# Kernel tuning notes

Measured on AMD Instinct MI355X. Metric: run time of the kernel, lower is better.

## Reference

```python
import jax, jax.numpy as jnp
import numpy as np

D, NH, NL, NP, DFF = 256, 8, 4, 4, 1024
HD = D // NH
SHAPES = np.array([[100, 152], [50, 76], [25, 38], [13, 19]], dtype=np.int64)
LV = int((SHAPES[:, 0] * SHAPES[:, 1]).sum())  # 20197


def setup_inputs() -> dict:
    key = jax.random.key(0)
    ks = iter(jax.random.split(key, 48))
    bs, Lq = 8, 300

    def w(shape, s=0.02):
        return jax.random.normal(next(ks), shape, jnp.float32) * s

    lsi = np.concatenate([[0], np.cumsum(SHAPES[:, 0] * SHAPES[:, 1])[:-1]]).astype(np.int64)
    return dict(
        tgt=w((bs, Lq, D), 1.0),
        query_pos=w((bs, Lq, D), 1.0),
        reference_points=jax.random.uniform(next(ks), (bs, Lq, NL, 2), jnp.float32),
        src=w((bs, LV, D), 1.0),
        in_proj_w=w((3 * D, D)), in_proj_b=jnp.zeros((3 * D,), jnp.float32),
        out_proj_w=w((D, D)), out_proj_b=jnp.zeros((D,), jnp.float32),
        samp_off_w=w((NH * NL * NP * 2, D)), samp_off_b=w((NH * NL * NP * 2,), 0.5),
        attn_w_w=w((NH * NL * NP, D)), attn_w_b=jnp.zeros((NH * NL * NP,), jnp.float32),
        value_proj_w=w((D, D)), value_proj_b=jnp.zeros((D,), jnp.float32),
        output_proj_w=w((D, D)), output_proj_b=jnp.zeros((D,), jnp.float32),
        lin1_w=w((DFF, D)), lin1_b=jnp.zeros((DFF,), jnp.float32),
        lin2_w=w((D, DFF)), lin2_b=jnp.zeros((D,), jnp.float32),
        norm1_w=jnp.ones((D,), jnp.float32), norm1_b=jnp.zeros((D,), jnp.float32),
        norm2_w=jnp.ones((D,), jnp.float32), norm2_b=jnp.zeros((D,), jnp.float32),
        norm3_w=jnp.ones((D,), jnp.float32), norm3_b=jnp.zeros((D,), jnp.float32),
        spatial_shapes=SHAPES,            # static numpy (shapes must be static)
        level_start_index=lsi,            # static numpy
        padding_mask=jnp.zeros((bs, LV), bool),
    )


def _ln(x, w, b):
    m = x.mean(-1, keepdims=True)
    v = ((x - m) ** 2).mean(-1, keepdims=True)
    return (x - m) * jax.lax.rsqrt(v + 1e-5) * w + b


def _bilinear(vflat, H_, W_, loc):
    # vflat: (b,h,H*W,d); loc: (b,h,q,p,2) normalized to [0,1]
    # matches F.grid_sample(align_corners=False, padding_mode='zeros')
    x = loc[..., 0] * W_ - 0.5
    y = loc[..., 1] * H_ - 0.5
    x0f, y0f = jnp.floor(x), jnp.floor(y)
    lx, ly = x - x0f, y - y0f
    x0, y0 = x0f.astype(jnp.int32), y0f.astype(jnp.int32)
    b, h, q, p = x0.shape

    def gather(ix, iy, wgt):
        valid = (ix >= 0) & (ix < W_) & (iy >= 0) & (iy < H_)
        idx = (jnp.clip(iy, 0, H_ - 1) * W_ + jnp.clip(ix, 0, W_ - 1)).reshape(b, h, q * p)
        g = jnp.take_along_axis(vflat, idx[..., None], axis=2)  # (b,h,q*p,d)
        return g * (wgt * valid).reshape(b, h, q * p, 1)

    out = (gather(x0, y0, (1 - lx) * (1 - ly)) + gather(x0 + 1, y0, lx * (1 - ly))
           + gather(x0, y0 + 1, (1 - lx) * ly) + gather(x0 + 1, y0 + 1, lx * ly))
    return out.reshape(b, h, q, p, -1)


def reference(tgt, query_pos, reference_points, src, in_proj_w, in_proj_b,
              out_proj_w, out_proj_b, samp_off_w, samp_off_b, attn_w_w, attn_w_b,
              value_proj_w, value_proj_b, output_proj_w, output_proj_b,
              lin1_w, lin1_b, lin2_w, lin2_b, norm1_w, norm1_b, norm2_w, norm2_b,
              norm3_w, norm3_b, spatial_shapes, level_start_index, padding_mask):
    bs, Lq, _ = tgt.shape
    ss = np.asarray(spatial_shapes)
    lsi = np.asarray(level_start_index)

    # ---- self attention (eval mode, dropout off) ----
    qk = tgt + query_pos
    qh = (qk @ in_proj_w[:D].T + in_proj_b[:D]).reshape(bs, Lq, NH, HD)
    kh = (qk @ in_proj_w[D:2 * D].T + in_proj_b[D:2 * D]).reshape(bs, Lq, NH, HD)
    vh = (tgt @ in_proj_w[2 * D:].T + in_proj_b[2 * D:]).reshape(bs, Lq, NH, HD)
    scores = jnp.einsum('bqhd,bkhd->bhqk', qh, kh) / jnp.sqrt(jnp.float32(HD))
    attn = jax.nn.softmax(scores, axis=-1)
    sa = jnp.einsum('bhqk,bkhd->bqhd', attn, vh).reshape(bs, Lq, D)
    sa = sa @ out_proj_w.T + out_proj_b
    x = _ln(tgt + sa, norm2_w, norm2_b)

    # ---- MSDeformAttn cross attention ----
    query = x + query_pos
    value = src @ value_proj_w.T + value_proj_b
    value = jnp.where(padding_mask[..., None], 0.0, value)
    value_t = value.reshape(bs, -1, NH, HD).transpose(0, 2, 1, 3)  # (b,h,Lv,d)

    offsets = (query @ samp_off_w.T + samp_off_b).reshape(bs, Lq, NH, NL, NP, 2)
    aw = jax.nn.softmax((query @ attn_w_w.T + attn_w_b).reshape(bs, Lq, NH, NL * NP), -1)
    aw = aw.reshape(bs, Lq, NH, NL, NP)
    norma = jnp.asarray(np.stack([ss[:, 1], ss[:, 0]], -1), jnp.float32)  # (NL,2)=[W,H]
    loc = reference_points[:, :, None, :, None, :] + offsets / norma[None, None, None, :, None, :]

    out = jnp.zeros((bs, Lq, NH, HD), value.dtype)
    for l in range(NL):
        H_, W_ = int(ss[l, 0]), int(ss[l, 1])
        s0 = int(lsi[l])
        vl = value_t[:, :, s0:s0 + H_ * W_]                    # (b,h,HW,d)
        ll = loc[:, :, :, l].transpose(0, 2, 1, 3, 4)          # (b,h,q,p,2)
        samp = _bilinear(vl, H_, W_, ll)                       # (b,h,q,p,d)
        out = out + jnp.einsum('bhqpd,bqhp->bqhd', samp, aw[:, :, :, l])
    ca = out.reshape(bs, Lq, D) @ output_proj_w.T + output_proj_b
    x = _ln(x + ca, norm1_w, norm1_b)

    # ---- FFN ----
    ffn = jax.nn.relu(x @ lin1_w.T + lin1_b) @ lin2_w.T + lin2_b
    x = _ln(x + ffn, norm3_w, norm3_b)
    return (x, loc, aw)
```

## Files before the change

kernel.cpp:

```cpp
#include <hip/hip_runtime.h>
#include <hip/hip_bf16.h>

#define D_ 256
#define NH_ 8
#define HD_ 32
#define NL_ 4
#define NP_ 4
#define DFF_ 1024
#define BS_ 8
#define LQ_ 300
#define LV_ 20197
#define NQ_ (BS_*LQ_)
#define NSRC_ (BS_*LV_*D_)

__device__ __forceinline__ float u2f(unsigned int u) {
    union { unsigned int i; float f; } v; v.i = u << 16; return v.f;
}
__device__ __forceinline__ float lo2f(unsigned int u) {
    union { unsigned int i; float f; } v; v.i = u << 16; return v.f;
}
__device__ __forceinline__ float hi2f(unsigned int u) {
    union { unsigned int i; float f; } v; v.i = u & 0xffff0000u; return v.f;
}
__device__ __forceinline__ unsigned short f2bf_bits(float f) {
    __hip_bfloat16 b = __float2bfloat16(f);
    union { __hip_bfloat16 b; unsigned short u; } v; v.b = b; return v.u;
}

#define DOT4(accum, wv, ap) do { \
    float4 _a = *(const float4*)(ap); \
    accum += wv.x*_a.x + wv.y*_a.y + wv.z*_a.z + wv.w*_a.w; } while(0)

__device__ __forceinline__ float block_sum256(float v, volatile float* red) {
#pragma unroll
    for (int off = 32; off; off >>= 1) v += __shfl_xor(v, off);
    __syncthreads();
    if ((threadIdx.x & 63) == 0) red[threadIdx.x >> 6] = v;
    __syncthreads();
    return red[0] + red[1] + red[2] + red[3];
}

__global__ __launch_bounds__(256) void cvt_bf16_kernel(
    const float* __restrict__ src, const float* __restrict__ wv,
    unsigned short* __restrict__ vbf, unsigned short* __restrict__ wbf)
{
    const int nsrc4 = NSRC_/4;
    const int total4 = nsrc4 + (D_*D_)/4;
    for (int i = blockIdx.x*256 + threadIdx.x; i < total4; i += gridDim.x*256) {
        float4 v;
        if (i < nsrc4) v = ((const float4*)src)[i];
        else           v = ((const float4*)wv)[i - nsrc4];
        ushort4 o;
        o.x = f2bf_bits(v.x); o.y = f2bf_bits(v.y);
        o.z = f2bf_bits(v.z); o.w = f2bf_bits(v.w);
        if (i < nsrc4) ((ushort4*)vbf)[i] = o;
        else           ((ushort4*)wbf)[i - nsrc4] = o;
    }
}

__global__ __launch_bounds__(256) void qkv_kernel(
    const float* __restrict__ tgt, const float* __restrict__ qp,
    const float* __restrict__ w, const float* __restrict__ bias,
    float* __restrict__ qh, float* __restrict__ kh, float* __restrict__ vh)
{
    __shared__ float arow[8][D_];
    const int t = threadIdx.x, m0 = blockIdx.x * 8, pass = blockIdx.y;
    for (int r = 0; r < 8; ++r) {
        float tv = tgt[(m0+r)*D_ + t];
        arow[r][t] = (pass == 2) ? tv : tv + qp[(m0+r)*D_ + t];
    }
    __syncthreads();
    const float4* w4 = (const float4*)(w + (pass*256 + t)*D_);
    float acc[8] = {0,0,0,0,0,0,0,0};
    for (int c = 0; c < 64; ++c) {
        float4 wv = w4[c];
#pragma unroll
        for (int r = 0; r < 8; ++r) DOT4(acc[r], wv, &arow[r][c*4]);
    }
    float bb = bias[pass*256 + t];
    float* dst = (pass == 0) ? qh : (pass == 1) ? kh : vh;
    for (int r = 0; r < 8; ++r) dst[(m0+r)*D_ + t] = acc[r] + bb;
}

__global__ __launch_bounds__(256) void attn_kernel(
    const float* __restrict__ qh, const float* __restrict__ kh,
    const float* __restrict__ vh, float* __restrict__ sa)
{
    __shared__ unsigned short khl[LQ_][HD_+2];
    __shared__ unsigned short vhl[LQ_][HD_+2];
    __shared__ float sc[4][LQ_];
    __shared__ float qbuf[4][HD_];
    const int b = blockIdx.x >> 3, h = blockIdx.x & 7, chunk = blockIdx.y;
    const int t = threadIdx.x, w = t >> 6, lane = t & 63;
    for (int i = t; i < LQ_*HD_; i += 256) {
        int kq = i >> 5, d = i & 31;
        khl[kq][d] = f2bf_bits(kh[(b*LQ_ + kq)*D_ + h*HD_ + d]);
        vhl[kq][d] = f2bf_bits(vh[(b*LQ_ + kq)*D_ + h*HD_ + d]);
    }
    __syncthreads();
    const float scale = 0.17677669529663687f;
    for (int qi = 0; qi < 15; ++qi) {
        const int q = chunk*60 + w*15 + qi;
        if (lane < HD_) qbuf[w][lane] = qh[(b*LQ_ + q)*D_ + h*HD_ + lane];
        __syncthreads();
        float qv[HD_];
#pragma unroll
        for (int d2 = 0; d2 < HD_; ++d2) qv[d2] = qbuf[w][d2];
        float mx = -1e30f;
        for (int k = lane; k < LQ_; k += 64) {
            float s = 0.f;
#pragma unroll
            for (int d2 = 0; d2 < HD_; ++d2) s += qv[d2]*u2f(khl[k][d2]);
            s *= scale;
            sc[w][k] = s;
            mx = fmaxf(mx, s);
        }
#pragma unroll
        for (int off = 32; off; off >>= 1) mx = fmaxf(mx, __shfl_xor(mx, off));
        float lsum = 0.f;
        for (int k = lane; k < LQ_; k += 64) {
            float e = __expf(sc[w][k] - mx);
            sc[w][k] = e; lsum += e;
        }
#pragma unroll
        for (int off = 32; off; off >>= 1) lsum += __shfl_xor(lsum, off);
        __syncthreads();
        const int d = lane & 31, half = lane >> 5;
        float acc = 0.f;
        for (int k = half*150; k < half*150 + 150; ++k) acc += sc[w][k]*u2f(vhl[k][d]);
        acc += __shfl_down(acc, 32);
        if (lane < 32) sa[(b*LQ_ + q)*D_ + h*HD_ + d] = acc / lsum;
        __syncthreads();
    }
}

__global__ __launch_bounds__(256) void proj_res_ln_kernel(
    const float* __restrict__ A, const float* __restrict__ W,
    const float* __restrict__ bias, const float* __restrict__ res,
    const float* __restrict__ gw, const float* __restrict__ gb,
    float* __restrict__ out)
{
    __shared__ float arow[8][D_];
    __shared__ float red[4];
    const int t = threadIdx.x, m0 = blockIdx.x * 8;
    for (int r = 0; r < 8; ++r) arow[r][t] = A[(m0+r)*D_ + t];
    __syncthreads();
    float acc[8] = {0,0,0,0,0,0,0,0};
    const float4* w4 = (const float4*)(W + t*D_);
    for (int c = 0; c < 64; ++c) {
        float4 wv = w4[c];
#pragma unroll
        for (int r = 0; r < 8; ++r) DOT4(acc[r], wv, &arow[r][c*4]);
    }
    const float bb = bias[t], gwv = gw[t], gbv = gb[t];
    for (int r = 0; r < 8; ++r) {
        int m = m0 + r;
        float v = acc[r] + bb + res[m*D_+t];
        float mean = block_sum256(v, red) * (1.0f/256.0f);
        float dv = v - mean;
        float var = block_sum256(dv*dv, red) * (1.0f/256.0f);
        out[m*D_+t] = dv * rsqrtf(var + 1e-5f) * gwv + gbv;
    }
}

__global__ __launch_bounds__(256) void samp_params_kernel(
    const float* __restrict__ x1, const float* __restrict__ qp,
    const float* __restrict__ so_w, const float* __restrict__ so_b,
    const float* __restrict__ aw_w, const float* __restrict__ aw_b,
    const float* __restrict__ refp,
    float* __restrict__ loc_out, float* __restrict__ aw_out)
{
    __shared__ float qrow[8][D_];
    __shared__ float logits[8][128];
    const int t = threadIdx.x, m0 = blockIdx.x * 8;
    for (int r = 0; r < 8; ++r)
        qrow[r][t] = x1[(m0+r)*D_ + t] + qp[(m0+r)*D_ + t];
    __syncthreads();
    {
        float acc[8] = {0,0,0,0,0,0,0,0};
        const float4* w4 = (const float4*)(so_w + t*D_);
        for (int c = 0; c < 64; ++c) {
            float4 wv = w4[c];
#pragma unroll
            for (int r = 0; r < 8; ++r) DOT4(acc[r], wv, &qrow[r][c*4]);
        }
        const float ob = so_b[t];
        const int c_ = t & 1, l_ = (t >> 3) & 3;
        float nrm;
        if (c_ == 0) nrm = (l_==0)?152.f:(l_==1)?76.f:(l_==2)?38.f:19.f;
        else         nrm = (l_==0)?100.f:(l_==1)?50.f:(l_==2)?25.f:13.f;
        for (int r = 0; r < 8; ++r) {
            int m = m0 + r;
            float off = acc[r] + ob;
            loc_out[m*256 + t] = refp[(m*NL_ + l_)*2 + c_] + off / nrm;
        }
    }
    if (t < 128) {
        float acc[8] = {0,0,0,0,0,0,0,0};
        const float4* w4 = (const float4*)(aw_w + t*D_);
        for (int c = 0; c < 64; ++c) {
            float4 wv = w4[c];
#pragma unroll
            for (int r = 0; r < 8; ++r) DOT4(acc[r], wv, &qrow[r][c*4]);
        }
        const float ab = aw_b[t];
        for (int r = 0; r < 8; ++r) logits[r][t] = acc[r] + ab;
    }
    __syncthreads();
    if (t < 128) {
        const int g0 = (t >> 4) << 4;
        for (int r = 0; r < 8; ++r) {
            float mx = -1e30f;
            for (int j = 0; j < 16; ++j) mx = fmaxf(mx, logits[r][g0+j]);
            float s = 0.f;
            for (int j = 0; j < 16; ++j) s += __expf(logits[r][g0+j] - mx);
            aw_out[(m0+r)*128 + t] = __expf(logits[r][t] - mx) / s;
        }
    }
}

__global__ __launch_bounds__(256) void samp_fuse_bf16_kernel(
    const unsigned short* __restrict__ vbf, const unsigned short* __restrict__ wbf,
    const float* __restrict__ vpb,
    const float* __restrict__ loc_f, const float* __restrict__ aw_f,
    float* __restrict__ vo)
{
    __shared__ float svec[NH_][D_];
    __shared__ int   cidx[128][4];
    __shared__ float cwt[128][4];
    __shared__ float wsum[NH_];
    const int m = blockIdx.x, t = threadIdx.x;
    const int b = m / LQ_;

    if (t < 128) {
        const int l = (t >> 2) & 3;
        const int HS[4] = {100,50,25,13}, WS[4] = {152,76,38,19}, S0[4] = {0,15200,19000,19950};
        const int Hh = HS[l], Ww = WS[l], s0 = S0[l];
        const float aw = aw_f[m*128 + t];
        const float x = loc_f[m*256 + 2*t]*Ww - 0.5f;
        const float y = loc_f[m*256 + 2*t + 1]*Hh - 0.5f;
        const float x0f = floorf(x), y0f = floorf(y);
        const int x0 = (int)x0f, y0 = (int)y0f;
        const float fx = x - x0f, fy = y - y0f;
        const int   cx[4] = {x0, x0+1, x0,   x0+1};
        const int   cy[4] = {y0, y0,   y0+1, y0+1};
        const float cw[4] = {(1.f-fx)*(1.f-fy), fx*(1.f-fy), (1.f-fx)*fy, fx*fy};
        float sw = 0.f;
#pragma unroll
        for (int j = 0; j < 4; ++j) {
            const bool valid = (cx[j] >= 0) & (cx[j] < Ww) & (cy[j] >= 0) & (cy[j] < Hh);
            cidx[t][j] = valid ? (s0 + cy[j]*Ww + cx[j]) : s0;
            float wv = valid ? aw*cw[j] : 0.f;
            cwt[t][j] = wv;
            sw += wv;
        }
#pragma unroll
        for (int off = 8; off; off >>= 1) sw += __shfl_xor(sw, off);
        if ((t & 15) == 0) wsum[t >> 4] = sw;
    }
    __syncthreads();

    const int hh = (t >> 7) * 4;
    const int c  = t & 127;
    const unsigned int* sb = (const unsigned int*)(vbf + (size_t)b*LV_*D_) + c;
#pragma unroll
    for (int h = hh; h < hh + 4; ++h) {
        float e0=0.f, e1=0.f, e2=0.f, e3=0.f;
        float o0=0.f, o1=0.f, o2=0.f, o3=0.f;
#pragma unroll 4
        for (int s = 0; s < 16; ++s) {
            const int base = h*16 + s;
            const int   i0 = cidx[base][0], i1 = cidx[base][1],
                        i2 = cidx[base][2], i3 = cidx[base][3];
            const float w0 = cwt[base][0], w1 = cwt[base][1],
                        w2 = cwt[base][2], w3 = cwt[base][3];
            const unsigned int u0 = sb[(size_t)i0*128];
            const unsigned int u1 = sb[(size_t)i1*128];
            const unsigned int u2 = sb[(size_t)i2*128];
            const unsigned int u3 = sb[(size_t)i3*128];
            e0 += w0*lo2f(u0); o0 += w0*hi2f(u0);
            e1 += w1*lo2f(u1); o1 += w1*hi2f(u1);
            e2 += w2*lo2f(u2); o2 += w2*hi2f(u2);
            e3 += w3*lo2f(u3); o3 += w3*hi2f(u3);
        }
        *(float2*)&svec[h][2*c] = make_float2((e0+e1)+(e2+e3), (o0+o1)+(o2+o3));
    }
    __syncthreads();

    const int h = t >> 5;
    const ushort4* w4 = (const ushort4*)(wbf + t*D_);
    float a = 0.f;
    for (int cc = 0; cc < 64; ++cc) {
        const ushort4 wq = w4[cc];
        const float4 sv = *(const float4*)&svec[h][cc*4];
        a += u2f(wq.x)*sv.x + u2f(wq.y)*sv.y + u2f(wq.z)*sv.z + u2f(wq.w)*sv.w;
    }
    vo[m*D_ + t] = a + vpb[t]*wsum[h];
}

__global__ __launch_bounds__(256) void samp_fuse_f32_kernel(
    const float* __restrict__ src, const float* __restrict__ Wv,
    const float* __restrict__ vpb,
    const float* __restrict__ loc_f, const float* __restrict__ aw_f,
    float* __restrict__ vo)
{
    __shared__ float svec[NH_][D_];
    __shared__ int   cidx[128][4];
    __shared__ float cwt[128][4];
    __shared__ float wsum[NH_];
    const int m = blockIdx.x, t = threadIdx.x;
    const int b = m / LQ_;

    if (t < 128) {
        const int l = (t >> 2) & 3;
        const int HS[4] = {100,50,25,13}, WS[4] = {152,76,38,19}, S0[4] = {0,15200,19000,19950};
        const int Hh = HS[l], Ww = WS[l], s0 = S0[l];
        const float aw = aw_f[m*128 + t];
        const float x = loc_f[m*256 + 2*t]*Ww - 0.5f;
        const float y = loc_f[m*256 + 2*t + 1]*Hh - 0.5f;
        const float x0f = floorf(x), y0f = floorf(y);
        const int x0 = (int)x0f, y0 = (int)y0f;
        const float fx = x - x0f, fy = y - y0f;
        const int   cx[4] = {x0, x0+1, x0,   x0+1};
        const int   cy[4] = {y0, y0,   y0+1, y0+1};
        const float cw[4] = {(1.f-fx)*(1.f-fy), fx*(1.f-fy), (1.f-fx)*fy, fx*fy};
        float sw = 0.f;
#pragma unroll
        for (int jj = 0; jj < 4; ++jj) {
            const bool valid = (cx[jj] >= 0) & (cx[jj] < Ww) & (cy[jj] >= 0) & (cy[jj] < Hh);
            cidx[t][jj] = valid ? (s0 + cy[jj]*Ww + cx[jj]) : s0;
            float wv = valid ? aw*cw[jj] : 0.f;
            cwt[t][jj] = wv;
            sw += wv;
        }
#pragma unroll
        for (int off = 8; off; off >>= 1) sw += __shfl_xor(sw, off);
        if ((t & 15) == 0) wsum[t >> 4] = sw;
    }
    __syncthreads();

    const float* sb = src + (size_t)b*LV_*D_ + t;
#pragma unroll
    for (int h = 0; h < NH_; ++h) {
        float a0 = 0.f, a1 = 0.f, a2 = 0.f, a3 = 0.f;
#pragma unroll 4
        for (int s = 0; s < 16; ++s) {
            const int base = h*16 + s;
            const int   i0 = cidx[base][0], i1 = cidx[base][1],
                        i2 = cidx[base][2], i3 = cidx[base][3];
            const float w0 = cwt[base][0], w1 = cwt[base][1],
                        w2 = cwt[base][2], w3 = cwt[base][3];
            a0 += w0 * sb[(size_t)i0*D_];
            a1 += w1 * sb[(size_t)i1*D_];
            a2 += w2 * sb[(size_t)i2*D_];
            a3 += w3 * sb[(size_t)i3*D_];
        }
        svec[h][t] = (a0 + a1) + (a2 + a3);
    }
    __syncthreads();

    const int h = t >> 5;
    const float4* w4 = (const float4*)(Wv + t*D_);
    float a = 0.f;
    for (int c = 0; c < 64; ++c) {
        float4 wv = w4[c];
        DOT4(a, wv, &svec[h][c*4]);
    }
    vo[m*D_ + t] = a + vpb[t]*wsum[h];
}

__global__ __launch_bounds__(256) void ffn1_kernel(
    const float* __restrict__ x2, const float* __restrict__ W1,
    const float* __restrict__ b1, float* __restrict__ hid)
{
    __shared__ float arow[8][D_];
    const int t = threadIdx.x, m0 = blockIdx.x * 8, cc = blockIdx.y;
    for (int r = 0; r < 8; ++r) arow[r][t] = x2[(m0+r)*D_ + t];
    __syncthreads();
    const int j = cc*256 + t;
    float acc[8] = {0,0,0,0,0,0,0,0};
    const float4* w4 = (const float4*)(W1 + j*D_);
    for (int c = 0; c < 64; ++c) {
        float4 wv = w4[c];
#pragma unroll
        for (int r = 0; r < 8; ++r) DOT4(acc[r], wv, &arow[r][c*4]);
    }
    const float bb = b1[j];
    for (int r = 0; r < 8; ++r) {
        float v = acc[r] + bb;
        hid[(m0+r)*DFF_ + j] = v > 0.f ? v : 0.f;
    }
}

__global__ __launch_bounds__(256) void ffn2_ln_kernel(
    const float* __restrict__ hid, const float* __restrict__ W2,
    const float* __restrict__ b2, const float* __restrict__ res,
    const float* __restrict__ gw, const float* __restrict__ gb,
    float* __restrict__ out)
{
    __shared__ float hrow[8][DFF_];
    __shared__ float red[4];
    const int t = threadIdx.x, m0 = blockIdx.x * 8;
    for (int i = t; i < 8*DFF_; i += 256)
        hrow[i >> 10][i & 1023] = hid[(m0 + (i >> 10))*DFF_ + (i & 1023)];
    __syncthreads();
    float acc[8] = {0,0,0,0,0,0,0,0};
    const float4* w4 = (const float4*)(W2 + t*DFF_);
    for (int c = 0; c < 256; ++c) {
        float4 wv = w4[c];
#pragma unroll
        for (int r = 0; r < 8; ++r) DOT4(acc[r], wv, &hrow[r][c*4]);
    }
    const float bb = b2[t], gwv = gw[t], gbv = gb[t];
    for (int r = 0; r < 8; ++r) {
        int m = m0 + r;
        float v = acc[r] + bb + res[m*D_+t];
        float mean = block_sum256(v, red) * (1.0f/256.0f);
        float dv = v - mean;
        float var = block_sum256(dv*dv, red) * (1.0f/256.0f);
        out[m*D_+t] = dv * rsqrtf(var + 1e-5f) * gwv + gbv;
    }
}

extern "C" void kernel_launch(void* const* d_in, const int* in_sizes, int n_in,
                              void* d_out, int out_size, void* d_ws, size_t ws_size,
                              hipStream_t stream) {
    (void)in_sizes; (void)n_in; (void)out_size;
    const float* tgt  = (const float*)d_in[0];
    const float* qpos = (const float*)d_in[1];
    const float* refp = (const float*)d_in[2];
    const float* srcp = (const float*)d_in[3];
    const float* ipw  = (const float*)d_in[4];
    const float* ipb  = (const float*)d_in[5];
    const float* opw  = (const float*)d_in[6];
    const float* opb  = (const float*)d_in[7];
    const float* sow  = (const float*)d_in[8];
    const float* sob  = (const float*)d_in[9];
    const float* aww  = (const float*)d_in[10];
    const float* awb  = (const float*)d_in[11];
    const float* vpw  = (const float*)d_in[12];
    const float* vpb  = (const float*)d_in[13];
    const float* outw = (const float*)d_in[14];
    const float* outb = (const float*)d_in[15];
    const float* l1w  = (const float*)d_in[16];
    const float* l1b  = (const float*)d_in[17];
    const float* l2w  = (const float*)d_in[18];
    const float* l2b  = (const float*)d_in[19];
    const float* n1w  = (const float*)d_in[20];
    const float* n1b  = (const float*)d_in[21];
    const float* n2w  = (const float*)d_in[22];
    const float* n2b  = (const float*)d_in[23];
    const float* n3w  = (const float*)d_in[24];
    const float* n3b  = (const float*)d_in[25];

    float* wsf = (float*)d_ws;
    float* qh   = wsf;
    float* kh   = wsf + 614400;
    float* vh   = wsf + 1228800;
    float* sa   = wsf + 1843200;
    float* x1   = wsf + 2457600;
    float* vo   = wsf + 3072000;
    float* x2   = wsf + 3686400;
    float* hid  = wsf + 4300800;
    unsigned short* vbf = (unsigned short*)(wsf + 6758400);
    unsigned short* wbf = (unsigned short*)(wsf + 6758400 + 20681728);
    const size_t need_bytes = (size_t)(6758400 + 20681728 + 32768) * 4;
    const bool use_bf16 = ws_size >= need_bytes;

    float* xout   = (float*)d_out;
    float* locout = xout + 614400;
    float* awout  = xout + 1228800;

    if (use_bf16)
        cvt_bf16_kernel<<<2048, 256, 0, stream>>>(srcp, vpw, vbf, wbf);
    qkv_kernel<<<dim3(NQ_/8, 3), 256, 0, stream>>>(tgt, qpos, ipw, ipb, qh, kh, vh);
    attn_kernel<<<dim3(BS_*NH_, 5), 256, 0, stream>>>(qh, kh, vh, sa);
    proj_res_ln_kernel<<<NQ_/8, 256, 0, stream>>>(sa, opw, opb, tgt, n2w, n2b, x1);
    samp_params_kernel<<<NQ_/8, 256, 0, stream>>>(x1, qpos, sow, sob, aww, awb, refp,
                                                  locout, awout);
    if (use_bf16)
        samp_fuse_bf16_kernel<<<NQ_, 256, 0, stream>>>(vbf, wbf, vpb, locout, awout, vo);
    else
        samp_fuse_f32_kernel<<<NQ_, 256, 0, stream>>>(srcp, vpw, vpb, locout, awout, vo);
    proj_res_ln_kernel<<<NQ_/8, 256, 0, stream>>>(vo, outw, outb, x1, n1w, n1b, x2);
    ffn1_kernel<<<dim3(NQ_/8, 4), 256, 0, stream>>>(x2, l1w, l1b, hid);
    ffn2_ln_kernel<<<NQ_/8, 256, 0, stream>>>(hid, l2w, l2b, x2, n3w, n3b, xout);
}
```

Measured before the change: 685.4 us.

## Split sampling from value projection, single-pass LayerNorm stats, drop attention barriers

```diff
diff --git a/kernel.cpp b/kernel.cpp
--- a/kernel.cpp
+++ b/kernel.cpp
@@ -31,15 +31,6 @@
     float4 _a = *(const float4*)(ap); \
     accum += wv.x*_a.x + wv.y*_a.y + wv.z*_a.z + wv.w*_a.w; } while(0)
 
-__device__ __forceinline__ float block_sum256(float v, volatile float* red) {
-#pragma unroll
-    for (int off = 32; off; off >>= 1) v += __shfl_xor(v, off);
-    __syncthreads();
-    if ((threadIdx.x & 63) == 0) red[threadIdx.x >> 6] = v;
-    __syncthreads();
-    return red[0] + red[1] + red[2] + red[3];
-}
-
 __global__ __launch_bounds__(256) void cvt_bf16_kernel(
     const float* __restrict__ src, const float* __restrict__ wv,
     unsigned short* __restrict__ vbf, unsigned short* __restrict__ wbf)
@@ -102,7 +93,6 @@
     for (int qi = 0; qi < 15; ++qi) {
         const int q = chunk*60 + w*15 + qi;
         if (lane < HD_) qbuf[w][lane] = qh[(b*LQ_ + q)*D_ + h*HD_ + lane];
-        __syncthreads();
         float qv[HD_];
 #pragma unroll
         for (int d2 = 0; d2 < HD_; ++d2) qv[d2] = qbuf[w][d2];
@@ -124,13 +114,11 @@
         }
 #pragma unroll
         for (int off = 32; off; off >>= 1) lsum += __shfl_xor(lsum, off);
-        __syncthreads();
         const int d = lane & 31, half = lane >> 5;
         float acc = 0.f;
         for (int k = half*150; k < half*150 + 150; ++k) acc += sc[w][k]*u2f(vhl[k][d]);
         acc += __shfl_down(acc, 32);
         if (lane < 32) sa[(b*LQ_ + q)*D_ + h*HD_ + d] = acc / lsum;
-        __syncthreads();
     }
 }
 
@@ -141,8 +129,9 @@
     float* __restrict__ out)
 {
     __shared__ float arow[8][D_];
-    __shared__ float red[4];
+    __shared__ float2 part[4][8];
     const int t = threadIdx.x, m0 = blockIdx.x * 8;
+    const int w = t >> 6, lane = t & 63;
     for (int r = 0; r < 8; ++r) arow[r][t] = A[(m0+r)*D_ + t];
     __syncthreads();
     float acc[8] = {0,0,0,0,0,0,0,0};
@@ -153,13 +142,25 @@
         for (int r = 0; r < 8; ++r) DOT4(acc[r], wv, &arow[r][c*4]);
     }
     const float bb = bias[t], gwv = gw[t], gbv = gb[t];
+    float v[8];
+#pragma unroll
     for (int r = 0; r < 8; ++r) {
-        int m = m0 + r;
-        float v = acc[r] + bb + res[m*D_+t];
-        float mean = block_sum256(v, red) * (1.0f/256.0f);
-        float dv = v - mean;
-        float var = block_sum256(dv*dv, red) * (1.0f/256.0f);
-        out[m*D_+t] = dv * rsqrtf(var + 1e-5f) * gwv + gbv;
+        v[r] = acc[r] + bb + res[(m0+r)*D_+t];
+        float s = v[r], ss = v[r]*v[r];
+#pragma unroll
+        for (int off = 32; off; off >>= 1) {
+            s += __shfl_xor(s, off); ss += __shfl_xor(ss, off);
+        }
+        if (lane == 0) part[w][r] = make_float2(s, ss);
+    }
+    __syncthreads();
+#pragma unroll
+    for (int r = 0; r < 8; ++r) {
+        float2 p0 = part[0][r], p1 = part[1][r], p2 = part[2][r], p3 = part[3][r];
+        float mean = (p0.x+p1.x+p2.x+p3.x) * (1.0f/256.0f);
+        float ex2  = (p0.y+p1.y+p2.y+p3.y) * (1.0f/256.0f);
+        float var  = ex2 - mean*mean;
+        out[(m0+r)*D_+t] = (v[r]-mean) * rsqrtf(var + 1e-5f) * gwv + gbv;
     }
 }
 
@@ -220,15 +221,12 @@
 }
 
 __global__ __launch_bounds__(256) void samp_fuse_bf16_kernel(
-    const unsigned short* __restrict__ vbf, const unsigned short* __restrict__ wbf,
-    const float* __restrict__ vpb,
+    const unsigned short* __restrict__ vbf,
     const float* __restrict__ loc_f, const float* __restrict__ aw_f,
-    float* __restrict__ vo)
-{
-    __shared__ float svec[NH_][D_];
+    float* __restrict__ svec_g, float* __restrict__ wsum_g)
+{
     __shared__ int   cidx[128][4];
     __shared__ float cwt[128][4];
-    __shared__ float wsum[NH_];
     const int m = blockIdx.x, t = threadIdx.x;
     const int b = m / LQ_;
 
@@ -256,7 +254,7 @@
         }
 #pragma unroll
         for (int off = 8; off; off >>= 1) sw += __shfl_xor(sw, off);
-        if ((t & 15) == 0) wsum[t >> 4] = sw;
+        if ((t & 15) == 0) wsum_g[m*NH_ + (t >> 4)] = sw;
     }
     __syncthreads();
 
@@ -283,19 +281,41 @@
             e2 += w2*lo2f(u2); o2 += w2*hi2f(u2);
             e3 += w3*lo2f(u3); o3 += w3*hi2f(u3);
         }
-        *(float2*)&svec[h][2*c] = make_float2((e0+e1)+(e2+e3), (o0+o1)+(o2+o3));
-    }
-    __syncthreads();
-
+        *(float2*)&svec_g[(size_t)m*(NH_*D_) + h*D_ + 2*c] =
+            make_float2((e0+e1)+(e2+e3), (o0+o1)+(o2+o3));
+    }
+}
+
+__global__ __launch_bounds__(256) void vproj_kernel(
+    const float* __restrict__ svec_g, const float* __restrict__ wsum_g,
+    const unsigned short* __restrict__ wbf, const float* __restrict__ vpb,
+    float* __restrict__ vo)
+{
+    __shared__ float sv[4][NH_*D_];
+    const int t = threadIdx.x, m0 = blockIdx.x * 4;
+    for (int i = t; i < 4*NH_*D_; i += 256)
+        sv[i >> 11][i & 2047] = svec_g[(size_t)m0*(NH_*D_) + i];
+    __syncthreads();
     const int h = t >> 5;
     const ushort4* w4 = (const ushort4*)(wbf + t*D_);
-    float a = 0.f;
-    for (int cc = 0; cc < 64; ++cc) {
-        const ushort4 wq = w4[cc];
-        const float4 sv = *(const float4*)&svec[h][cc*4];
-        a += u2f(wq.x)*sv.x + u2f(wq.y)*sv.y + u2f(wq.z)*sv.z + u2f(wq.w)*sv.w;
-    }
-    vo[m*D_ + t] = a + vpb[t]*wsum[h];
+    float a0 = 0.f, a1 = 0.f, a2 = 0.f, a3 = 0.f;
+    for (int c = 0; c < 64; ++c) {
+        const ushort4 wq = w4[c];
+        const float wx = u2f(wq.x), wy = u2f(wq.y), wz = u2f(wq.z), ww = u2f(wq.w);
+        const float4 s0 = *(const float4*)&sv[0][h*D_ + c*4];
+        const float4 s1 = *(const float4*)&sv[1][h*D_ + c*4];
+        const float4 s2 = *(const float4*)&sv[2][h*D_ + c*4];
+        const float4 s3 = *(const float4*)&sv[3][h*D_ + c*4];
+        a0 += wx*s0.x + wy*s0.y + wz*s0.z + ww*s0.w;
+        a1 += wx*s1.x + wy*s1.y + wz*s1.z + ww*s1.w;
+        a2 += wx*s2.x + wy*s2.y + wz*s2.z + ww*s2.w;
+        a3 += wx*s3.x + wy*s3.y + wz*s3.z + ww*s3.w;
+    }
+    const float bb = vpb[t];
+    vo[(size_t)(m0+0)*D_ + t] = a0 + bb*wsum_g[(m0+0)*NH_ + h];
+    vo[(size_t)(m0+1)*D_ + t] = a1 + bb*wsum_g[(m0+1)*NH_ + h];
+    vo[(size_t)(m0+2)*D_ + t] = a2 + bb*wsum_g[(m0+2)*NH_ + h];
+    vo[(size_t)(m0+3)*D_ + t] = a3 + bb*wsum_g[(m0+3)*NH_ + h];
 }
 
 __global__ __launch_bounds__(256) void samp_fuse_f32_kernel(
@@ -399,8 +419,9 @@
     float* __restrict__ out)
 {
     __shared__ float hrow[8][DFF_];
-    __shared__ float red[4];
+    __shared__ float2 part[4][8];
     const int t = threadIdx.x, m0 = blockIdx.x * 8;
+    const int w = t >> 6, lane = t & 63;
     for (int i = t; i < 8*DFF_; i += 256)
         hrow[i >> 10][i & 1023] = hid[(m0 + (i >> 10))*DFF_ + (i & 1023)];
     __syncthreads();
@@ -412,13 +433,25 @@
         for (int r = 0; r < 8; ++r) DOT4(acc[r], wv, &hrow[r][c*4]);
     }
     const float bb = b2[t], gwv = gw[t], gbv = gb[t];
+    float v[8];
+#pragma unroll
     for (int r = 0; r < 8; ++r) {
-        int m = m0 + r;
-        float v = acc[r] + bb + res[m*D_+t];
-        float mean = block_sum256(v, red) * (1.0f/256.0f);
-        float dv = v - mean;
-        float var = block_sum256(dv*dv, red) * (1.0f/256.0f);
-        out[m*D_+t] = dv * rsqrtf(var + 1e-5f) * gwv + gbv;
+        v[r] = acc[r] + bb + res[(m0+r)*D_+t];
+        float s = v[r], ss = v[r]*v[r];
+#pragma unroll
+        for (int off = 32; off; off >>= 1) {
+            s += __shfl_xor(s, off); ss += __shfl_xor(ss, off);
+        }
+        if (lane == 0) part[w][r] = make_float2(s, ss);
+    }
+    __syncthreads();
+#pragma unroll
+    for (int r = 0; r < 8; ++r) {
+        float2 p0 = part[0][r], p1 = part[1][r], p2 = part[2][r], p3 = part[3][r];
+        float mean = (p0.x+p1.x+p2.x+p3.x) * (1.0f/256.0f);
+        float ex2  = (p0.y+p1.y+p2.y+p3.y) * (1.0f/256.0f);
+        float var  = ex2 - mean*mean;
+        out[(m0+r)*D_+t] = (v[r]-mean) * rsqrtf(var + 1e-5f) * gwv + gbv;
     }
 }
 
@@ -464,7 +497,9 @@
     float* hid  = wsf + 4300800;
     unsigned short* vbf = (unsigned short*)(wsf + 6758400);
     unsigned short* wbf = (unsigned short*)(wsf + 6758400 + 20681728);
-    const size_t need_bytes = (size_t)(6758400 + 20681728 + 32768) * 4;
+    float* svec_g = wsf + 6758400 + 20681728 + 32768;
+    float* wsum_g = svec_g + 4915200;
+    const size_t need_bytes = (size_t)(6758400 + 20681728 + 32768 + 4915200 + 19200) * 4;
     const bool use_bf16 = ws_size >= need_bytes;
 
     float* xout   = (float*)d_out;
@@ -478,10 +513,12 @@
     proj_res_ln_kernel<<<NQ_/8, 256, 0, stream>>>(sa, opw, opb, tgt, n2w, n2b, x1);
     samp_params_kernel<<<NQ_/8, 256, 0, stream>>>(x1, qpos, sow, sob, aww, awb, refp,
                                                   locout, awout);
-    if (use_bf16)
-        samp_fuse_bf16_kernel<<<NQ_, 256, 0, stream>>>(vbf, wbf, vpb, locout, awout, vo);
-    else
+    if (use_bf16) {
+        samp_fuse_bf16_kernel<<<NQ_, 256, 0, stream>>>(vbf, locout, awout, svec_g, wsum_g);
+        vproj_kernel<<<NQ_/4, 256, 0, stream>>>(svec_g, wsum_g, wbf, vpb, vo);
+    } else {
         samp_fuse_f32_kernel<<<NQ_, 256, 0, stream>>>(srcp, vpw, vpb, locout, awout, vo);
+    }
     proj_res_ln_kernel<<<NQ_/8, 256, 0, stream>>>(vo, outw, outb, x1, n1w, n1b, x2);
     ffn1_kernel<<<dim3(NQ_/8, 4), 256, 0, stream>>>(x2, l1w, l1b, hid);
     ffn2_ln_kernel<<<NQ_/8, 256, 0, stream>>>(hid, l2w, l2b, x2, n3w, n3b, xout);
```

After: 654.7 us. 4.5% less time.
